# Optimization experiments

Hardware: AMD Instinct MI355X
Metric: run time of the kernel (lower is better)

The kernel has to match this reference:

```python
import jax, jax.numpy as jnp
import numpy as np

N_NODES = 100000
N_EDGES = 1600000
IN_C, HID, OUT_C = 64, 128, 64


def setup_inputs() -> dict:
    key = jax.random.key(0)
    ks = jax.random.split(key, 10)
    x = jax.random.normal(ks[0], (N_NODES, IN_C), dtype=jnp.float32)
    edge_index = jax.random.randint(ks[1], (2, N_EDGES), 0, N_NODES, dtype=jnp.int32)

    def lin(k, fan_in, fan_out):
        kw, kb = jax.random.split(k)
        bound = 1.0 / np.sqrt(fan_in)
        W = jax.random.uniform(kw, (fan_in, fan_out), minval=-bound, maxval=bound, dtype=jnp.float32)
        b = jax.random.uniform(kb, (fan_out,), minval=-bound, maxval=bound, dtype=jnp.float32)
        return W, b

    W1a, b1a = lin(ks[2], IN_C, HID)
    W1b, b1b = lin(ks[3], HID, HID)
    W2a, b2a = lin(ks[4], HID, HID)
    W2b, b2b = lin(ks[5], HID, OUT_C)
    return {"x": x, "edge_index": edge_index,
            "W1a": W1a, "b1a": b1a, "W1b": W1b, "b1b": b1b,
            "W2a": W2a, "b2a": b2a, "W2b": W2b, "b2b": b2b}


def _gin_conv(h, src, dst, n_nodes, Wa, ba, Wb, bb):
    # sum-aggregate neighbor features: agg[i] = sum_{(j->i) in E} h[j]
    agg = jax.ops.segment_sum(h[src], dst, num_segments=n_nodes)
    z = agg + h  # (1 + eps) * x with eps = 0 (PyG default)
    z = jax.nn.relu(z @ Wa + ba)
    return z @ Wb + bb


def reference(x, edge_index, W1a, b1a, W1b, b1b, W2a, b2a, W2b, b2b):
    src, dst = edge_index[0], edge_index[1]
    n = x.shape[0]
    h = _gin_conv(x, src, dst, n, W1a, b1a, W1b, b1b)
    h = jax.nn.relu(h)
    # dropout is identity in eval mode (training=False)
    out = _gin_conv(h, src, dst, n, W2a, b2a, W2b, b2b)
    return out
```

## Files before the change

### kernel.cpp

```cpp
#include <hip/hip_runtime.h>
#include <hip/hip_bf16.h>


#define CB   512
#define NBMX 256
#define CAP  48
#define FL   16

typedef short  bf16x8 __attribute__((ext_vector_type(8)));
typedef float  f32x4  __attribute__((ext_vector_type(4)));

__device__ inline float bf2f(unsigned short u) {
    unsigned int t = ((unsigned int)u) << 16;
    return __builtin_bit_cast(float, t);
}
__device__ inline unsigned short f2bf(float f) {
    unsigned int u = __builtin_bit_cast(unsigned int, f);
    u += 0x7fffu + ((u >> 16) & 1u);
    return (unsigned short)(u >> 16);
}

__global__ __launch_bounds__(256) void prep_k(
    const float* __restrict__ x, unsigned short* __restrict__ xb, int n8,
    const float* __restrict__ W1a, const float* __restrict__ W1b,
    const float* __restrict__ W2a, const float* __restrict__ W2b,
    unsigned short* __restrict__ T1a, unsigned short* __restrict__ T1b,
    unsigned short* __restrict__ T2a, unsigned short* __restrict__ T2b)
{
    int b = blockIdx.x;
    if (b < 192) {
        int idx = b * 256 + threadIdx.x;
        const float* W; unsigned short* T; int K, N;
        if (idx < 8192)        { W = W1a; T = T1a; K = 64;  N = 128; }
        else if (idx < 24576)  { idx -= 8192;  W = W1b; T = T1b; K = 128; N = 128; }
        else if (idx < 40960)  { idx -= 24576; W = W2a; T = T2a; K = 128; N = 128; }
        else if (idx < 49152)  { idx -= 40960; W = W2b; T = T2b; K = 128; N = 64; }
        else return;
        int n = idx / K, k = idx - n * K;
        T[idx] = f2bf(W[(size_t)k * N + n]);
    } else {
        int i = (b - 192) * 256 + threadIdx.x;
        if (i >= n8) return;
        const float4* p = reinterpret_cast<const float4*>(x + (size_t)i * 8);
        float4 a = p[0], c = p[1];
        union { unsigned short us[8]; uint4 v; } o;
        o.us[0] = f2bf(a.x); o.us[1] = f2bf(a.y); o.us[2] = f2bf(a.z); o.us[3] = f2bf(a.w);
        o.us[4] = f2bf(c.x); o.us[5] = f2bf(c.y); o.us[6] = f2bf(c.z); o.us[7] = f2bf(c.w);
        *reinterpret_cast<uint4*>(xb + (size_t)i * 8) = o.v;
    }
}

__global__ __launch_bounds__(256) void bhist_k(
    const int* __restrict__ dst, int* __restrict__ bcnt, int n_edges, int nbuck)
{
    __shared__ int lh[NBMX];
    const int tid = threadIdx.x;
    for (int b = tid; b < nbuck; b += 256) lh[b] = 0;
    __syncthreads();
    const int e4 = n_edges >> 2;
    const int stride = gridDim.x * 256;
    for (int i4 = blockIdx.x * 256 + tid; i4 < e4; i4 += stride) {
        int4 dv = reinterpret_cast<const int4*>(dst)[i4];
        atomicAdd(&lh[dv.x / CB], 1);
        atomicAdd(&lh[dv.y / CB], 1);
        atomicAdd(&lh[dv.z / CB], 1);
        atomicAdd(&lh[dv.w / CB], 1);
    }
    if (blockIdx.x == 0 && tid < (n_edges & 3))
        atomicAdd(&lh[dst[e4 * 4 + tid] / CB], 1);
    __syncthreads();
    for (int b = tid; b < nbuck; b += 256) {
        int v = lh[b];
        if (v) atomicAdd(&bcnt[b], v);
    }
}

__global__ __launch_bounds__(256) void bscan_k(
    const int* __restrict__ bcnt, int* __restrict__ boffs,
    int* __restrict__ gcur, int nbuck)
{
    __shared__ int s[256];
    const int tid = threadIdx.x;
    int v = (tid < nbuck) ? bcnt[tid] : 0;
    s[tid] = v; __syncthreads();
    #pragma unroll
    for (int d = 1; d < 256; d <<= 1) {
        int t = (tid >= d) ? s[tid - d] : 0;
        __syncthreads();
        s[tid] += t;
        __syncthreads();
    }
    if (tid < nbuck) {
        int excl = s[tid] - v;
        boffs[tid] = excl;
        gcur[tid] = excl;
        if (tid == nbuck - 1) boffs[nbuck] = s[tid];
    }
}

template<bool VEC4>
__global__ __launch_bounds__(256) void bucket_p1_k(
    const int* __restrict__ src, const int* __restrict__ dst,
    int* __restrict__ gcur, unsigned int* __restrict__ tmp,
    int n_edges, int nb)
{
    __shared__ unsigned int stage[NBMX][CAP];
    __shared__ int scnt[NBMX];
    const int tid = threadIdx.x;
    for (int b = tid; b < nb; b += 256) scnt[b] = 0;
    __syncthreads();

    const int e4total = n_edges >> 2;
    const int stride = gridDim.x * 256;
    const int iters = (e4total + stride - 1) / stride;

    for (int it = 0; it < iters; ++it) {
        int i4 = it * stride + blockIdx.x * 256 + tid;
        if (i4 < e4total) {
            int s4[4], d4[4];
            if constexpr (VEC4) {
                int4 sv = reinterpret_cast<const int4*>(src)[i4];
                int4 dv = reinterpret_cast<const int4*>(dst)[i4];
                s4[0]=sv.x; s4[1]=sv.y; s4[2]=sv.z; s4[3]=sv.w;
                d4[0]=dv.x; d4[1]=dv.y; d4[2]=dv.z; d4[3]=dv.w;
            } else {
                #pragma unroll
                for (int j = 0; j < 4; ++j) { s4[j]=src[i4*4+j]; d4[j]=dst[i4*4+j]; }
            }
            #pragma unroll
            for (int j = 0; j < 4; ++j) {
                int dd = d4[j];
                int b = dd / CB;
                unsigned int entry = (unsigned int)s4[j] | ((unsigned int)(dd - b * CB) << 20);
                int slot = atomicAdd(&scnt[b], 1);
                if (slot < CAP) stage[b][slot] = entry;
                else { int p = atomicAdd(&gcur[b], 1); tmp[p] = entry; }
            }
        }
        __syncthreads();
        if (tid < nb) {
            int m = scnt[tid]; if (m > CAP) m = CAP;
            while (m >= FL) {
                int base = atomicAdd(&gcur[tid], FL);
                #pragma unroll
                for (int q = 0; q < FL; ++q)
                    tmp[base + q] = stage[tid][m - FL + q];
                m -= FL;
            }
            scnt[tid] = m;
        }
        __syncthreads();
    }
    if (tid < nb) {
        int m = scnt[tid]; if (m > CAP) m = CAP;
        if (m > 0) {
            int base = atomicAdd(&gcur[tid], m);
            for (int q = 0; q < m; ++q) tmp[base + q] = stage[tid][q];
        }
    }
    if (blockIdx.x == 0 && tid < (n_edges & 3)) {
        int e = e4total * 4 + tid;
        int dd = dst[e];
        int b = dd / CB;
        unsigned int entry = (unsigned int)src[e] | ((unsigned int)(dd - b * CB) << 20);
        int p = atomicAdd(&gcur[b], 1);
        tmp[p] = entry;
    }
}

__global__ __launch_bounds__(256) void bucket_csr_k(
    const unsigned int* __restrict__ tmp, const int* __restrict__ boffs,
    int* __restrict__ offs, int* __restrict__ cnt, int* __restrict__ eidx,
    int n_nodes)
{
    __shared__ int lcnt[CB];
    __shared__ int lcur[CB];
    __shared__ int ssum[256];
    const int b = blockIdx.x;
    const int tid = threadIdx.x;
    const int node0 = b * CB;
    const int nn = min(CB, n_nodes - node0);
    const int lo = boffs[b], hi = boffs[b + 1];

    for (int i = tid; i < CB; i += 256) lcnt[i] = 0;
    __syncthreads();
    for (int i = lo + tid; i < hi; i += 256)
        atomicAdd(&lcnt[tmp[i] >> 20], 1);
    __syncthreads();

    int a0 = lcnt[tid * 2], a1 = lcnt[tid * 2 + 1];
    int tsum = a0 + a1;
    ssum[tid] = tsum; __syncthreads();
    #pragma unroll
    for (int d = 1; d < 256; d <<= 1) {
        int t = (tid >= d) ? ssum[tid - d] : 0;
        __syncthreads();
        ssum[tid] += t;
        __syncthreads();
    }
    int run = ssum[tid] - tsum;

    lcur[tid * 2]     = run;
    lcur[tid * 2 + 1] = run + a0;
    int g0 = node0 + tid * 2;
    if (tid * 2 < nn)     { offs[g0]     = lo + run;      cnt[g0]     = a0; }
    if (tid * 2 + 1 < nn) { offs[g0 + 1] = lo + run + a0; cnt[g0 + 1] = a1; }
    __syncthreads();

    for (int i = lo + tid; i < hi; i += 256) {
        unsigned int v = tmp[i];
        int p = atomicAdd(&lcur[v >> 20], 1);
        eidx[lo + p] = (int)(v & 0xFFFFFu);
    }
}

__global__ __launch_bounds__(256) void hist_k(
    const int* __restrict__ dst, int* __restrict__ cnt, int n_edges)
{
    int e = blockIdx.x * 256 + threadIdx.x;
    if (e < n_edges) atomicAdd(&cnt[dst[e]], 1);
}

__global__ __launch_bounds__(256) void scan_block_k(
    const int* __restrict__ cnt, int* __restrict__ offs, int* __restrict__ bsum, int n)
{
    __shared__ int s[256];
    const int tid = threadIdx.x;
    const int base = blockIdx.x * 2048 + tid * 8;
    int v[8]; int tsum = 0;
    #pragma unroll
    for (int j = 0; j < 8; ++j) {
        int idx = base + j;
        v[j] = (idx < n) ? cnt[idx] : 0;
        tsum += v[j];
    }
    s[tid] = tsum; __syncthreads();
    #pragma unroll
    for (int d = 1; d < 256; d <<= 1) {
        int t = (tid >= d) ? s[tid - d] : 0;
        __syncthreads();
        s[tid] += t;
        __syncthreads();
    }
    int run = s[tid] - tsum;
    #pragma unroll
    for (int j = 0; j < 8; ++j) {
        int idx = base + j;
        if (idx < n) offs[idx] = run;
        run += v[j];
    }
    if (tid == 255) bsum[blockIdx.x] = s[255];
}

__global__ __launch_bounds__(256) void scan_bsum_k(int* __restrict__ bsum, int nb)
{
    __shared__ int s[256];
    const int tid = threadIdx.x;
    int v = (tid < nb) ? bsum[tid] : 0;
    s[tid] = v; __syncthreads();
    #pragma unroll
    for (int d = 1; d < 256; d <<= 1) {
        int t = (tid >= d) ? s[tid - d] : 0;
        __syncthreads();
        s[tid] += t;
        __syncthreads();
    }
    if (tid < nb) bsum[tid] = s[tid] - v;
}

__global__ __launch_bounds__(256) void scan_add_k(
    int* __restrict__ offs, int* __restrict__ cur, const int* __restrict__ bsum, int n)
{
    const int b = bsum[blockIdx.x];
    const int base = blockIdx.x * 2048 + threadIdx.x * 8;
    #pragma unroll
    for (int j = 0; j < 8; ++j) {
        int idx = base + j;
        if (idx < n) { int o = offs[idx] + b; offs[idx] = o; cur[idx] = o; }
    }
}

__global__ __launch_bounds__(256) void fill_k(
    const int* __restrict__ src, const int* __restrict__ dst,
    int* __restrict__ cur, int* __restrict__ eidx, int n_edges)
{
    int e = blockIdx.x * 256 + threadIdx.x;
    if (e < n_edges) {
        int p = atomicAdd(&cur[dst[e]], 1);
        eidx[p] = src[e];
    }
}

template<int C>
__global__ __launch_bounds__(256) void gather_agg_k(
    const unsigned short* __restrict__ h, const int* __restrict__ offs,
    const int* __restrict__ cnt, const int* __restrict__ eidx,
    unsigned short* __restrict__ A, int n_nodes)
{
    constexpr int TPN = C / 8;
    constexpr int NPB = 256 / TPN;
    const int node = blockIdx.x * NPB + threadIdx.x / TPN;
    const int lane = threadIdx.x % TPN;
    if (node >= n_nodes) return;
    const size_t coff = (size_t)lane * 8;

    float acc[8];
    {
        uint4 v = *reinterpret_cast<const uint4*>(h + (size_t)node * C + coff);
        const unsigned short* u = (const unsigned short*)&v;
        #pragma unroll
        for (int j = 0; j < 8; ++j) acc[j] = bf2f(u[j]);
    }
    const int beg = offs[node], end = beg + cnt[node];
    int p = beg;
    for (; p + 4 <= end; p += 4) {
        int s0 = eidx[p], s1 = eidx[p + 1], s2 = eidx[p + 2], s3 = eidx[p + 3];
        uint4 v0 = *reinterpret_cast<const uint4*>(h + (size_t)s0 * C + coff);
        uint4 v1 = *reinterpret_cast<const uint4*>(h + (size_t)s1 * C + coff);
        uint4 v2 = *reinterpret_cast<const uint4*>(h + (size_t)s2 * C + coff);
        uint4 v3 = *reinterpret_cast<const uint4*>(h + (size_t)s3 * C + coff);
        const unsigned short* u0 = (const unsigned short*)&v0;
        const unsigned short* u1 = (const unsigned short*)&v1;
        const unsigned short* u2 = (const unsigned short*)&v2;
        const unsigned short* u3 = (const unsigned short*)&v3;
        #pragma unroll
        for (int j = 0; j < 8; ++j)
            acc[j] += (bf2f(u0[j]) + bf2f(u1[j])) + (bf2f(u2[j]) + bf2f(u3[j]));
    }
    if (p + 2 <= end) {
        int s0 = eidx[p], s1 = eidx[p + 1];
        uint4 v0 = *reinterpret_cast<const uint4*>(h + (size_t)s0 * C + coff);
        uint4 v1 = *reinterpret_cast<const uint4*>(h + (size_t)s1 * C + coff);
        const unsigned short* u0 = (const unsigned short*)&v0;
        const unsigned short* u1 = (const unsigned short*)&v1;
        #pragma unroll
        for (int j = 0; j < 8; ++j) acc[j] += bf2f(u0[j]) + bf2f(u1[j]);
        p += 2;
    }
    if (p < end) {
        uint4 v0 = *reinterpret_cast<const uint4*>(h + (size_t)eidx[p] * C + coff);
        const unsigned short* u0 = (const unsigned short*)&v0;
        #pragma unroll
        for (int j = 0; j < 8; ++j) acc[j] += bf2f(u0[j]);
    }
    union { unsigned short us[8]; uint4 v; } o;
    #pragma unroll
    for (int j = 0; j < 8; ++j) o.us[j] = f2bf(acc[j]);
    *reinterpret_cast<uint4*>(A + (size_t)node * C + coff) = o.v;
}

template<int K1, int N2, bool RELU_OUT, bool OUT_BF16>
__global__ __launch_bounds__(256) void mlp_mfma_k(
    const unsigned short* __restrict__ Ain,
    const unsigned short* __restrict__ WTa,
    const float* __restrict__ ba,
    const unsigned short* __restrict__ WTb,
    const float* __restrict__ bb,
    void* __restrict__ outp, int n_nodes)
{
    constexpr int KS1 = K1 / 32;
    constexpr int NT2 = N2 / 16;
    static_assert(128 * K1 <= 128 * 128, "sA fits sAM");
    static_assert(128 * N2 * (OUT_BF16 ? 2 : 4) <= 128 * 128 * 2, "out stage fits sAM");

    __shared__ __align__(16) unsigned short sAM[128 * 128];
    __shared__ __align__(16) unsigned short sWa[128 * K1];
    __shared__ __align__(16) unsigned short sWb[N2 * 128];

    const int tid = threadIdx.x;
    const int wave = tid >> 6, lane = tid & 63;
    const int rc = lane & 15;
    const int kg = lane >> 4;
    const int rowBlock = blockIdx.x * 128;

    {
        constexpr int CPR = K1 / 8;
        #pragma unroll
        for (int f = tid; f < 128 * CPR; f += 256) {
            int r = f / CPR, c = f - r * CPR;
            uint4 v = make_uint4(0u, 0u, 0u, 0u);
            int gr = rowBlock + r;
            if (gr < n_nodes)
                v = *reinterpret_cast<const uint4*>(Ain + (size_t)gr * K1 + c * 8);
            int byte = r * (K1 * 2) + ((c * 16) ^ ((r & 7) << 4));
            *reinterpret_cast<uint4*>((char*)sAM + byte) = v;
        }
    }
    {
        constexpr int CPR = K1 / 8;
        #pragma unroll
        for (int f = tid; f < 128 * CPR; f += 256) {
            int r = f / CPR, c = f - r * CPR;
            uint4 v = *reinterpret_cast<const uint4*>(WTa + (size_t)r * K1 + c * 8);
            int byte = r * (K1 * 2) + ((c * 16) ^ ((r & 7) << 4));
            *reinterpret_cast<uint4*>((char*)sWa + byte) = v;
        }
    }
    {
        #pragma unroll
        for (int f = tid; f < N2 * 16; f += 256) {
            int r = f / 16, c = f - r * 16;
            uint4 v = *reinterpret_cast<const uint4*>(WTb + (size_t)r * 128 + c * 8);
            int byte = r * 256 + ((c * 16) ^ ((r & 7) << 4));
            *reinterpret_cast<uint4*>((char*)sWb + byte) = v;
        }
    }
    __syncthreads();

    bf16x8 af[2][KS1];
    #pragma unroll
    for (int rt = 0; rt < 2; ++rt)
        #pragma unroll
        for (int ks = 0; ks < KS1; ++ks) {
            int r = wave * 32 + rt * 16 + rc;
            int byte = r * (K1 * 2) + (((ks * 32 + kg * 8) * 2) ^ ((r & 7) << 4));
            af[rt][ks] = *reinterpret_cast<const bf16x8*>((const char*)sAM + byte);
        }
    __syncthreads();

    f32x4 acc1[2][8];
    #pragma unroll
    for (int rt = 0; rt < 2; ++rt)
        #pragma unroll
        for (int n = 0; n < 8; ++n) acc1[rt][n] = (f32x4){0.f, 0.f, 0.f, 0.f};
    #pragma unroll
    for (int n = 0; n < 8; ++n) {
        int c = n * 16 + rc;
        #pragma unroll
        for (int ks = 0; ks < KS1; ++ks) {
            int byte = c * (K1 * 2) + (((ks * 32 + kg * 8) * 2) ^ ((c & 7) << 4));
            bf16x8 bfr = *reinterpret_cast<const bf16x8*>((const char*)sWa + byte);
            #pragma unroll
            for (int rt = 0; rt < 2; ++rt)
                acc1[rt][n] = __builtin_amdgcn_mfma_f32_16x16x32_bf16(
                    af[rt][ks], bfr, acc1[rt][n], 0, 0, 0);
        }
    }
    #pragma unroll
    for (int n = 0; n < 8; ++n) {
        int c = n * 16 + rc;
        float bias = ba[c];
        #pragma unroll
        for (int rt = 0; rt < 2; ++rt)
            #pragma unroll
            for (int i = 0; i < 4; ++i) {
                int r = wave * 32 + rt * 16 + kg * 4 + i;
                float v = fmaxf(acc1[rt][n][i] + bias, 0.f);
                int byte = r * 256 + ((c * 2) ^ ((r & 7) << 4));
                *reinterpret_cast<unsigned short*>((char*)sAM + byte) = f2bf(v);
            }
    }
    __syncthreads();

    bf16x8 mf[2][4];
    #pragma unroll
    for (int rt = 0; rt < 2; ++rt)
        #pragma unroll
        for (int ks = 0; ks < 4; ++ks) {
            int r = wave * 32 + rt * 16 + rc;
            int byte = r * 256 + (((ks * 32 + kg * 8) * 2) ^ ((r & 7) << 4));
            mf[rt][ks] = *reinterpret_cast<const bf16x8*>((const char*)sAM + byte);
        }
    f32x4 acc2[2][NT2];
    #pragma unroll
    for (int rt = 0; rt < 2; ++rt)
        #pragma unroll
        for (int n = 0; n < NT2; ++n) acc2[rt][n] = (f32x4){0.f, 0.f, 0.f, 0.f};
    #pragma unroll
    for (int n = 0; n < NT2; ++n) {
        int c = n * 16 + rc;
        #pragma unroll
        for (int ks = 0; ks < 4; ++ks) {
            int byte = c * 256 + (((ks * 32 + kg * 8) * 2) ^ ((c & 7) << 4));
            bf16x8 bfr = *reinterpret_cast<const bf16x8*>((const char*)sWb + byte);
            #pragma unroll
            for (int rt = 0; rt < 2; ++rt)
                acc2[rt][n] = __builtin_amdgcn_mfma_f32_16x16x32_bf16(
                    mf[rt][ks], bfr, acc2[rt][n], 0, 0, 0);
        }
    }
    __syncthreads();

    if constexpr (OUT_BF16) {
        #pragma unroll
        for (int n = 0; n < NT2; ++n) {
            int c = n * 16 + rc;
            float bias = bb[c];
            #pragma unroll
            for (int rt = 0; rt < 2; ++rt)
                #pragma unroll
                for (int i = 0; i < 4; ++i) {
                    int r = wave * 32 + rt * 16 + kg * 4 + i;
                    float v = acc2[rt][n][i] + bias;
                    if (RELU_OUT) v = fmaxf(v, 0.f);
                    sAM[r * N2 + c] = f2bf(v);
                }
        }
        __syncthreads();
        unsigned short* out = (unsigned short*)outp;
        constexpr int CPR = N2 / 8;
        #pragma unroll
        for (int f = tid; f < 128 * CPR; f += 256) {
            int r = f / CPR, c = f - r * CPR;
            int gr = rowBlock + r;
            if (gr < n_nodes)
                *reinterpret_cast<uint4*>(out + (size_t)gr * N2 + c * 8) =
                    *reinterpret_cast<const uint4*>(sAM + r * N2 + c * 8);
        }
    } else {
        float* sOut = reinterpret_cast<float*>(sAM);
        #pragma unroll
        for (int n = 0; n < NT2; ++n) {
            int c = n * 16 + rc;
            float bias = bb[c];
            #pragma unroll
            for (int rt = 0; rt < 2; ++rt)
                #pragma unroll
                for (int i = 0; i < 4; ++i) {
                    int r = wave * 32 + rt * 16 + kg * 4 + i;
                    float v = acc2[rt][n][i] + bias;
                    if (RELU_OUT) v = fmaxf(v, 0.f);
                    sOut[r * N2 + c] = v;
                }
        }
        __syncthreads();
        float* out = (float*)outp;
        constexpr int CPR = N2 / 4;
        #pragma unroll
        for (int f = tid; f < 128 * CPR; f += 256) {
            int r = f / CPR, c = f - r * CPR;
            int gr = rowBlock + r;
            if (gr < n_nodes)
                *reinterpret_cast<float4*>(out + (size_t)gr * N2 + c * 4) =
                    *reinterpret_cast<const float4*>(sOut + r * N2 + c * 4);
        }
    }
}

extern "C" void kernel_launch(void* const* d_in, const int* in_sizes, int n_in,
                              void* d_out, int out_size, void* d_ws, size_t ws_size,
                              hipStream_t stream)
{
    const float* x   = (const float*)d_in[0];
    const int*   ei  = (const int*)d_in[1];
    const float* W1a = (const float*)d_in[2];
    const float* b1a = (const float*)d_in[3];
    const float* W1b = (const float*)d_in[4];
    const float* b1b = (const float*)d_in[5];
    const float* W2a = (const float*)d_in[6];
    const float* b2a = (const float*)d_in[7];
    const float* W2b = (const float*)d_in[8];
    const float* b2b = (const float*)d_in[9];

    const int n_nodes = in_sizes[0] / 64;
    const int n_edges = in_sizes[1] / 2;
    const int* src = ei;
    const int* dst = ei + n_edges;

    char* ws = (char*)d_ws;
    size_t o = 0;
    auto alloc = [&](size_t bytes) -> char* {
        char* p = ws + o;
        o += (bytes + 255) & ~(size_t)255;
        return p;
    };
    unsigned short* A    = (unsigned short*)alloc((size_t)n_nodes * 128 * 2);
    unsigned short* h    = (unsigned short*)alloc((size_t)n_nodes * 128 * 2);
    unsigned short* xb   = (unsigned short*)alloc((size_t)n_nodes * 64 * 2);
    int* eidx = (int*)alloc((size_t)n_edges * 4);
    unsigned int* tmp = (unsigned int*)alloc((size_t)n_edges * 4);
    int* cnt  = (int*)alloc((size_t)n_nodes * 4);
    int* offs = (int*)alloc((size_t)n_nodes * 4);
    int* cur  = (int*)alloc((size_t)n_nodes * 4);
    int* bsum = (int*)alloc(256 * 4);
    int* gcur = (int*)alloc(NBMX * 4);
    int* bcnt = (int*)alloc((NBMX + 1) * 4);
    int* boffs = (int*)alloc((NBMX + 1) * 4);
    unsigned short* WT1a = (unsigned short*)alloc(64 * 128 * 2);
    unsigned short* WT1b = (unsigned short*)alloc(128 * 128 * 2);
    unsigned short* WT2a = (unsigned short*)alloc(128 * 128 * 2);
    unsigned short* WT2b = (unsigned short*)alloc(128 * 64 * 2);

    const int mlp_grid = (n_nodes + 127) / 128;
    const int egrid = (n_edges + 255) / 256;
    const int nbuck = (n_nodes + CB - 1) / CB;

    prep_k<<<192 + (n_nodes * 8 + 255) / 256, 256, 0, stream>>>(
        x, xb, n_nodes * 8, W1a, W1b, W2a, W2b, WT1a, WT1b, WT2a, WT2b);

    if (nbuck <= NBMX && n_nodes < (1 << 20)) {
        hipMemsetAsync(bcnt, 0, (NBMX + 1) * sizeof(int), stream);
        bhist_k<<<128, 256, 0, stream>>>(dst, bcnt, n_edges, nbuck);
        bscan_k<<<1, 256, 0, stream>>>(bcnt, boffs, gcur, nbuck);
        const bool vec4 = ((n_edges & 3) == 0);
        if (vec4)
            bucket_p1_k<true><<<256, 256, 0, stream>>>(src, dst, gcur, tmp, n_edges, nbuck);
        else
            bucket_p1_k<false><<<256, 256, 0, stream>>>(src, dst, gcur, tmp, n_edges, nbuck);
        bucket_csr_k<<<nbuck, 256, 0, stream>>>(tmp, boffs, offs, cnt, eidx, n_nodes);
    } else {
        hipMemsetAsync(cnt, 0, (size_t)n_nodes * sizeof(int), stream);
        hist_k<<<egrid, 256, 0, stream>>>(dst, cnt, n_edges);
        const int nb = (n_nodes + 2047) / 2048;
        scan_block_k<<<nb, 256, 0, stream>>>(cnt, offs, bsum, n_nodes);
        scan_bsum_k<<<1, 256, 0, stream>>>(bsum, nb);
        scan_add_k<<<nb, 256, 0, stream>>>(offs, cur, bsum, n_nodes);
        fill_k<<<egrid, 256, 0, stream>>>(src, dst, cur, eidx, n_edges);
    }

    gather_agg_k<64><<<(n_nodes + 31) / 32, 256, 0, stream>>>(
        xb, offs, cnt, eidx, A, n_nodes);
    mlp_mfma_k<64, 128, true, true><<<mlp_grid, 256, 0, stream>>>(
        A, WT1a, b1a, WT1b, b1b, h, n_nodes);

    gather_agg_k<128><<<(n_nodes + 15) / 16, 256, 0, stream>>>(
        h, offs, cnt, eidx, A, n_nodes);
    mlp_mfma_k<128, 64, false, false><<<mlp_grid, 256, 0, stream>>>(
        A, WT2a, b2a, WT2b, b2b, d_out, n_nodes);
}
```

Before: 209.1 us.

## Fuse bucket histogram into prep kernel and parallelize bucket flush writes

The bucket histogram kernel is folded into the prep kernel as 64 extra blocks, which removes one launch and lets the histogram run alongside the weight and feature conversion. In bucket_p1_k the per-bucket flush, where one thread copied the staged entries serially, becomes a two-phase scheme. One thread reserves the output range for each bucket with a single atomic, then 16 threads per bucket copy the entries in parallel. This adds an extra barrier per iteration and a little shared memory, and gives the histogram only 64 blocks instead of 128.

```diff
diff --git a/kernel.cpp b/kernel.cpp
--- a/kernel.cpp
+++ b/kernel.cpp
@@ -25,11 +25,35 @@
     const float* __restrict__ W1a, const float* __restrict__ W1b,
     const float* __restrict__ W2a, const float* __restrict__ W2b,
     unsigned short* __restrict__ T1a, unsigned short* __restrict__ T1b,
-    unsigned short* __restrict__ T2a, unsigned short* __restrict__ T2b)
-{
-    int b = blockIdx.x;
-    if (b < 192) {
-        int idx = b * 256 + threadIdx.x;
+    unsigned short* __restrict__ T2a, unsigned short* __restrict__ T2b,
+    const int* __restrict__ dst, int* __restrict__ bcnt,
+    int hist_edges, int nbuck)
+{
+    __shared__ int lh[NBMX];
+    const int b = blockIdx.x;
+    const int tid = threadIdx.x;
+    if (b < 64) {
+        if (hist_edges == 0) return;
+        for (int i = tid; i < nbuck; i += 256) lh[i] = 0;
+        __syncthreads();
+        const int e4 = hist_edges >> 2;
+        const int stride = 64 * 256;
+        for (int i4 = b * 256 + tid; i4 < e4; i4 += stride) {
+            int4 dv = reinterpret_cast<const int4*>(dst)[i4];
+            atomicAdd(&lh[dv.x / CB], 1);
+            atomicAdd(&lh[dv.y / CB], 1);
+            atomicAdd(&lh[dv.z / CB], 1);
+            atomicAdd(&lh[dv.w / CB], 1);
+        }
+        if (b == 0 && tid < (hist_edges & 3))
+            atomicAdd(&lh[dst[e4 * 4 + tid] / CB], 1);
+        __syncthreads();
+        for (int i = tid; i < nbuck; i += 256) {
+            int v = lh[i];
+            if (v) atomicAdd(&bcnt[i], v);
+        }
+    } else if (b < 256) {
+        int idx = (b - 64) * 256 + tid;
         const float* W; unsigned short* T; int K, N;
         if (idx < 8192)        { W = W1a; T = T1a; K = 64;  N = 128; }
         else if (idx < 24576)  { idx -= 8192;  W = W1b; T = T1b; K = 128; N = 128; }
@@ -39,7 +63,7 @@
         int n = idx / K, k = idx - n * K;
         T[idx] = f2bf(W[(size_t)k * N + n]);
     } else {
-        int i = (b - 192) * 256 + threadIdx.x;
+        int i = (b - 256) * 256 + tid;
         if (i >= n8) return;
         const float4* p = reinterpret_cast<const float4*>(x + (size_t)i * 8);
         float4 a = p[0], c = p[1];
@@ -50,31 +74,6 @@
     }
 }
 
-__global__ __launch_bounds__(256) void bhist_k(
-    const int* __restrict__ dst, int* __restrict__ bcnt, int n_edges, int nbuck)
-{
-    __shared__ int lh[NBMX];
-    const int tid = threadIdx.x;
-    for (int b = tid; b < nbuck; b += 256) lh[b] = 0;
-    __syncthreads();
-    const int e4 = n_edges >> 2;
-    const int stride = gridDim.x * 256;
-    for (int i4 = blockIdx.x * 256 + tid; i4 < e4; i4 += stride) {
-        int4 dv = reinterpret_cast<const int4*>(dst)[i4];
-        atomicAdd(&lh[dv.x / CB], 1);
-        atomicAdd(&lh[dv.y / CB], 1);
-        atomicAdd(&lh[dv.z / CB], 1);
-        atomicAdd(&lh[dv.w / CB], 1);
-    }
-    if (blockIdx.x == 0 && tid < (n_edges & 3))
-        atomicAdd(&lh[dst[e4 * 4 + tid] / CB], 1);
-    __syncthreads();
-    for (int b = tid; b < nbuck; b += 256) {
-        int v = lh[b];
-        if (v) atomicAdd(&bcnt[b], v);
-    }
-}
-
 __global__ __launch_bounds__(256) void bscan_k(
     const int* __restrict__ bcnt, int* __restrict__ boffs,
     int* __restrict__ gcur, int nbuck)
@@ -106,6 +105,9 @@
 {
     __shared__ unsigned int stage[NBMX][CAP];
     __shared__ int scnt[NBMX];
+    __shared__ int fbase[NBMX];
+    __shared__ short fcnt[NBMX];
+    __shared__ short foff[NBMX];
     const int tid = threadIdx.x;
     for (int b = tid; b < nb; b += 256) scnt[b] = 0;
     __syncthreads();
@@ -140,14 +142,21 @@
         __syncthreads();
         if (tid < nb) {
             int m = scnt[tid]; if (m > CAP) m = CAP;
-            while (m >= FL) {
-                int base = atomicAdd(&gcur[tid], FL);
-                #pragma unroll
-                for (int q = 0; q < FL; ++q)
-                    tmp[base + q] = stage[tid][m - FL + q];
-                m -= FL;
+            int nf = m & ~(FL - 1);
+            fcnt[tid] = (short)nf;
+            foff[tid] = (short)(m - nf);
+            fbase[tid] = nf ? atomicAdd(&gcur[tid], nf) : 0;
+            scnt[tid] = m - nf;
+        }
+        __syncthreads();
+        for (int bb = tid >> 4; bb < nb; bb += 16) {
+            int q = tid & 15;
+            int nf = fcnt[bb];
+            if (nf) {
+                int off = foff[bb], base = fbase[bb];
+                for (int u = q; u < nf; u += 16)
+                    tmp[base + u] = stage[bb][off + u];
             }
-            scnt[tid] = m;
         }
         __syncthreads();
     }
@@ -584,13 +593,14 @@
     const int mlp_grid = (n_nodes + 127) / 128;
     const int egrid = (n_edges + 255) / 256;
     const int nbuck = (n_nodes + CB - 1) / CB;
-
-    prep_k<<<192 + (n_nodes * 8 + 255) / 256, 256, 0, stream>>>(
-        x, xb, n_nodes * 8, W1a, W1b, W2a, W2b, WT1a, WT1b, WT2a, WT2b);
-
-    if (nbuck <= NBMX && n_nodes < (1 << 20)) {
-        hipMemsetAsync(bcnt, 0, (NBMX + 1) * sizeof(int), stream);
-        bhist_k<<<128, 256, 0, stream>>>(dst, bcnt, n_edges, nbuck);
+    const bool bucket_path = (nbuck <= NBMX && n_nodes < (1 << 20));
+
+    hipMemsetAsync(bcnt, 0, (NBMX + 1) * sizeof(int), stream);
+    prep_k<<<256 + (n_nodes * 8 + 255) / 256, 256, 0, stream>>>(
+        x, xb, n_nodes * 8, W1a, W1b, W2a, W2b, WT1a, WT1b, WT2a, WT2b,
+        dst, bcnt, bucket_path ? n_edges : 0, nbuck);
+
+    if (bucket_path) {
         bscan_k<<<1, 256, 0, stream>>>(bcnt, boffs, gcur, nbuck);
         const bool vec4 = ((n_edges & 3) == 0);
         if (vec4)
```

Measured after the change: 218.0 us. 1.04x slower.
